# Kernel optimization log

Hardware: AMD Instinct MI355X
Metric: run time of the kernel (lower is better)

Reference implementation:

```python
import jax, jax.numpy as jnp
import numpy as np

N, E = 20000, 320000
IN, HID, R, HEADS = 128, 256, 4, 4
C = HID // HEADS  # per-head dim


def setup_inputs() -> dict:
    key = jax.random.key(0)
    ks = jax.random.split(key, 20)
    g = lambda k, s, sc=0.05: jax.random.normal(k, s, jnp.float32) * sc
    return {
        'x': g(ks[0], (N, IN), 1.0),
        'edge_index': jax.random.randint(ks[1], (2, E), 0, N),
        'edge_type': jax.random.randint(ks[2], (E,), 0, R),
        'h_prev': g(ks[3], (N, HID), 1.0),
        # RGCN layer 1: relation weights, root weight, bias
        'W1': g(ks[4], (R, IN, HID)), 'root1': g(ks[5], (IN, HID)), 'b1': jnp.zeros((HID,), jnp.float32),
        # RGCN layer 2
        'W2': g(ks[6], (R, HID, HID)), 'root2': g(ks[7], (HID, HID)), 'b2': jnp.zeros((HID,), jnp.float32),
        # TransformerConv linears (query/key/value/skip), each Linear(HID, HEADS*C)
        'Wq': g(ks[8], (HID, HID)), 'bq': jnp.zeros((HID,), jnp.float32),
        'Wk': g(ks[9], (HID, HID)), 'bk': jnp.zeros((HID,), jnp.float32),
        'Wv': g(ks[10], (HID, HID)), 'bv': jnp.zeros((HID,), jnp.float32),
        'Wskip': g(ks[11], (HID, HID)), 'bskip': jnp.zeros((HID,), jnp.float32),
        # GRUCell (torch layout: [3*HID, in], gates ordered r, z, n)
        'W_ih': g(ks[12], (3 * HID, HID)), 'b_ih': jnp.zeros((3 * HID,), jnp.float32),
        'W_hh': g(ks[13], (3 * HID, HID)), 'b_hh': jnp.zeros((3 * HID,), jnp.float32),
    }


def rgcn(x, src, dst, etype, W, Wroot, b):
    # PyG RGCNConv: out_i = x_i @ Wroot + b + sum_r mean_{j in N_r(i)} x_j @ W_r
    n = x.shape[0]
    out = x @ Wroot + b
    xs = x[src]  # [E, F_in]
    for r in range(W.shape[0]):  # small fixed relation count
        mask = (etype == r).astype(x.dtype)  # [E]
        msg = (xs @ W[r]) * mask[:, None]  # [E, F_out]
        agg = jax.ops.segment_sum(msg, dst, num_segments=n)
        cnt = jax.ops.segment_sum(mask, dst, num_segments=n)
        out = out + agg / jnp.maximum(cnt, 1.0)[:, None]
    return out


def transformer_conv(x, src, dst, Wq, bq, Wk, bk, Wv, bv, Wskip, bskip):
    # PyG TransformerConv, concat=True, root_weight=True
    n = x.shape[0]
    q = (x @ Wq + bq).reshape(n, HEADS, C)
    k = (x @ Wk + bk).reshape(n, HEADS, C)
    v = (x @ Wv + bv).reshape(n, HEADS, C)
    score = jnp.einsum('ehc,ehc->eh', q[dst], k[src]) * (1.0 / np.sqrt(C))  # [E, H]
    smax = jax.ops.segment_max(score, dst, num_segments=n)  # [N, H]
    ex = jnp.exp(score - smax[dst])
    denom = jax.ops.segment_sum(ex, dst, num_segments=n)
    alpha = ex / jnp.maximum(denom[dst], 1e-16)  # edge softmax per dst node
    out = jax.ops.segment_sum(alpha[:, :, None] * v[src], dst, num_segments=n)  # [N, H, C]
    return out.reshape(n, HEADS * C) + x @ Wskip + bskip


def gru_cell(xi, h, W_ih, b_ih, W_hh, b_hh):
    gi = xi @ W_ih.T + b_ih
    gh = h @ W_hh.T + b_hh
    ir, iz, inn = jnp.split(gi, 3, axis=1)
    hr, hz, hn = jnp.split(gh, 3, axis=1)
    r = jax.nn.sigmoid(ir + hr)
    z = jax.nn.sigmoid(iz + hz)
    nw = jnp.tanh(inn + r * hn)
    return (1.0 - z) * nw + z * h


def reference(x, edge_index, edge_type, h_prev, W1, root1, b1, W2, root2, b2,
              Wq, bq, Wk, bk, Wv, bv, Wskip, bskip, W_ih, b_ih, W_hh, b_hh):
    src, dst = edge_index[0], edge_index[1]
    h = jax.nn.relu(rgcn(x, src, dst, edge_type, W1, root1, b1))
    h = jax.nn.relu(rgcn(h, src, dst, edge_type, W2, root2, b2))
    h = transformer_conv(h, src, dst, Wq, bq, Wk, bk, Wv, bv, Wskip, bskip)
    h = gru_cell(h, h_prev, W_ih, b_ih, W_hh, b_hh)
    return h
```

## Files before the change

kernel.cpp:

```cpp
#include <hip/hip_runtime.h>
#include <hip/hip_bf16.h>
#include <stdint.h>

#define N_NODES 20000
#define E_EDGES 320000
#define IN_F    128
#define HIDF    256
#define R_REL   4
#define NRKEYS  (N_NODES*R_REL)
#define SCAN_BLOCKS 80

typedef __attribute__((ext_vector_type(8))) short  short8;
typedef __attribute__((ext_vector_type(4))) float  floatx4;

__device__ __forceinline__ float bf2f(__hip_bfloat16 v){ return __bfloat162float(v); }
__device__ __forceinline__ __hip_bfloat16 f2bf(float v){ return __float2bfloat16(v); }
__device__ __forceinline__ float bfbits2f(unsigned short u){ return __uint_as_float(((unsigned)u)<<16); }
__device__ __forceinline__ unsigned short f2bfbits(float v){
    __hip_bfloat16 h = __float2bfloat16(v);
    return *(unsigned short*)&h;
}
__device__ __forceinline__ unsigned pack_bf2(float a, float b){
    return (unsigned)f2bfbits(a) | ((unsigned)f2bfbits(b) << 16);
}

__device__ __forceinline__ void gload_lds16(const void* g, void* l)
{
    __builtin_amdgcn_global_load_lds((const __attribute__((address_space(1))) void*)g,
                                     (__attribute__((address_space(3))) void*)l, 16, 0, 0);
}

template<int N>
__device__ __forceinline__ void wait_vm()
{
    if constexpr (N == 0)      asm volatile("s_waitcnt vmcnt(0)" ::: "memory");
    else if constexpr (N == 3) asm volatile("s_waitcnt vmcnt(3)" ::: "memory");
    else if constexpr (N == 4) asm volatile("s_waitcnt vmcnt(4)" ::: "memory");
    else if constexpr (N == 5) asm volatile("s_waitcnt vmcnt(5)" ::: "memory");
    else if constexpr (N == 8) asm volatile("s_waitcnt vmcnt(8)" ::: "memory");
    else                       asm volatile("s_waitcnt vmcnt(0)" ::: "memory");
}

__device__ __forceinline__ int2 xcd_swizzle()
{
    int gx = gridDim.x, gy = gridDim.y;
    int nwg = gx * gy;
    int lin = blockIdx.x + gx * blockIdx.y;
    int q = nwg >> 3, r = nwg & 7;
    int k = lin & 7, i = lin >> 3;
    int j = (k < r ? k*(q+1) : r*(q+1) + (k-r)*q) + i;
    return make_int2(j / gy, j % gy);
}

__global__ void count_kernel(const int* __restrict__ ei, const int* __restrict__ et,
                             int* __restrict__ cnt)
{
    int e = blockIdx.x*256 + threadIdx.x;
    if (e >= E_EDGES) return;
    int dst = ei[E_EDGES + e];
    atomicAdd(&cnt[dst*R_REL + et[e]], 1);
}

__global__ __launch_bounds__(1024) void scan_reduce_kernel(const int* __restrict__ cnt,
                                                           int* __restrict__ blocksum)
{
    int ix = blockIdx.x*1024 + threadIdx.x;
    int v = (ix < NRKEYS) ? cnt[ix] : 0;
    #pragma unroll
    for (int o=32;o>0;o>>=1) v += __shfl_xor(v, o, 64);
    __shared__ int wsum[16];
    int wave = threadIdx.x >> 6, lane = threadIdx.x & 63;
    if (lane == 0) wsum[wave] = v;
    __syncthreads();
    if (threadIdx.x == 0) {
        int s = 0;
        #pragma unroll
        for (int w=0;w<16;w++) s += wsum[w];
        blocksum[blockIdx.x] = s;
    }
}

__global__ __launch_bounds__(128) void scan_sums_kernel(const int* __restrict__ blocksum,
                                                        int* __restrict__ blockoff)
{
    __shared__ int s[128];
    int t = threadIdx.x;
    int v = (t < SCAN_BLOCKS) ? blocksum[t] : 0;
    s[t] = v; __syncthreads();
    for (int off=1; off<128; off<<=1) {
        int u = (t>=off) ? s[t-off] : 0;
        __syncthreads();
        s[t] += u;
        __syncthreads();
    }
    if (t < SCAN_BLOCKS) blockoff[t] = s[t] - v;
}

__global__ __launch_bounds__(1024) void scan_apply_kernel(const int* __restrict__ cnt,
                                                          const int* __restrict__ blockoff,
                                                          int* __restrict__ row_ptr,
                                                          int* __restrict__ cursor)
{
    __shared__ int s[1024];
    int t = threadIdx.x;
    int ix = blockIdx.x*1024 + t;
    int v = (ix < NRKEYS) ? cnt[ix] : 0;
    s[t] = v; __syncthreads();
    for (int off=1; off<1024; off<<=1) {
        int u = (t>=off) ? s[t-off] : 0;
        __syncthreads();
        s[t] += u;
        __syncthreads();
    }
    if (ix < NRKEYS) {
        int excl = blockoff[blockIdx.x] + s[t] - v;
        row_ptr[ix] = excl;
        cursor[ix]  = excl;
        if (ix == NRKEYS-1) row_ptr[NRKEYS] = excl + v;
    }
}

__global__ void fill_kernel(const int* __restrict__ ei, const int* __restrict__ et,
                            int* __restrict__ cursor, int* __restrict__ csr_src)
{
    int e = blockIdx.x*256 + threadIdx.x;
    if (e >= E_EDGES) return;
    int src = ei[e];
    int dst = ei[E_EDGES + e];
    int key = dst*R_REL + et[e];
    int pos = atomicAdd(&cursor[key], 1);
    csr_src[pos] = src;
}

__global__ void make_b1t(const float* __restrict__ root1,
                         const float* __restrict__ W1,
                         __hip_bfloat16* __restrict__ B1t)
{
    int idx = blockIdx.x*256 + threadIdx.x;
    if (idx >= 256*640) return;
    int n = idx / 640, k = idx % 640;
    float v;
    if (k < 128) v = root1[k*256 + n];
    else         v = W1[(k-128)*256 + n];
    B1t[idx] = f2bf(v);
}

__global__ void make_b2t(const float* __restrict__ root2,
                         const float* __restrict__ W2,
                         __hip_bfloat16* __restrict__ B2t)
{
    int idx = blockIdx.x*256 + threadIdx.x;
    if (idx >= 256*1280) return;
    int n = idx / 1280, k = idx % 1280;
    float v;
    if (k < 256) v = root2[k*256 + n];
    else         v = W2[(k-256)*256 + n];
    B2t[idx] = f2bf(v);
}

__global__ void make_b3t(const float* __restrict__ Wq, const float* __restrict__ Wk,
                         const float* __restrict__ Wv, const float* __restrict__ Wsk,
                         const float* __restrict__ bq, const float* __restrict__ bk,
                         const float* __restrict__ bv, const float* __restrict__ bsk,
                         __hip_bfloat16* __restrict__ B3t, float* __restrict__ bias3)
{
    int idx = blockIdx.x*256 + threadIdx.x;
    if (idx >= 1024*256) return;
    int n = idx / 256, k = idx % 256;
    int g = n >> 8, nn = n & 255;
    const float* W = (g==0)?Wq:(g==1)?Wk:(g==2)?Wv:Wsk;
    B3t[idx] = f2bf(W[k*256 + nn]);
    if (k == 0) {
        const float* B = (g==0)?bq:(g==1)?bk:(g==2)?bv:bsk;
        bias3[n] = B[nn];
    }
}

__global__ void cvt_f32_bf16(const float* __restrict__ in, __hip_bfloat16* __restrict__ out, int n)
{
    int i = blockIdx.x*256 + threadIdx.x;
    if (i < n) out[i] = f2bf(in[i]);
}

__global__ __launch_bounds__(256) void agg1_kernel(const float* __restrict__ x,
                                                   const int* __restrict__ row_ptr,
                                                   const int* __restrict__ csr_src,
                                                   __hip_bfloat16* __restrict__ A1)
{
    int b = blockIdx.x*4 + (threadIdx.x >> 6);
    int lane = threadIdx.x & 63;
    int i = b >> 2, r = b & 3;
    int e0 = row_ptr[b], e1 = row_ptr[b+1];
    float sx0=0.f,sy0=0.f, sx1=0.f,sy1=0.f, sx2=0.f,sy2=0.f, sx3=0.f,sy3=0.f;
    int e = e0;
    for (; e+4 <= e1; e += 4) {
        int i0=csr_src[e], i1=csr_src[e+1], i2=csr_src[e+2], i3=csr_src[e+3];
        float2 v0 = *(const float2*)(x + (size_t)i0*IN_F + lane*2);
        float2 v1 = *(const float2*)(x + (size_t)i1*IN_F + lane*2);
        float2 v2 = *(const float2*)(x + (size_t)i2*IN_F + lane*2);
        float2 v3 = *(const float2*)(x + (size_t)i3*IN_F + lane*2);
        sx0+=v0.x; sy0+=v0.y; sx1+=v1.x; sy1+=v1.y;
        sx2+=v2.x; sy2+=v2.y; sx3+=v3.x; sy3+=v3.y;
    }
    for (; e < e1; e++) {
        int i0 = csr_src[e];
        float2 v = *(const float2*)(x + (size_t)i0*IN_F + lane*2);
        sx0+=v.x; sy0+=v.y;
    }
    float sx = (sx0+sx1)+(sx2+sx3);
    float sy = (sy0+sy1)+(sy2+sy3);
    float inv = (e1>e0) ? 1.f/(float)(e1-e0) : 0.f;
    *(unsigned*)(A1 + (size_t)i*640 + 128 + r*128 + lane*2) = pack_bf2(sx*inv, sy*inv);
    if (r == 0) {
        float2 v = *(const float2*)(x + (size_t)i*IN_F + lane*2);
        *(unsigned*)(A1 + (size_t)i*640 + lane*2) = pack_bf2(v.x, v.y);
    }
}

__global__ __launch_bounds__(256) void agg2_kernel(const int* __restrict__ row_ptr,
                                                   const int* __restrict__ csr_src,
                                                   __hip_bfloat16* __restrict__ A2)
{
    int b = blockIdx.x*4 + (threadIdx.x >> 6);
    int lane = threadIdx.x & 63;
    int i = b >> 2, r = b & 3;
    int e0 = row_ptr[b], e1 = row_ptr[b+1];
    float a0=0.f,a1=0.f,a2=0.f,a3=0.f;
    float b0=0.f,b1=0.f,b2=0.f,b3=0.f;
    float c0=0.f,c1=0.f,c2=0.f,c3=0.f;
    float d0=0.f,d1=0.f,d2=0.f,d3=0.f;
    int e = e0;
    for (; e+4 <= e1; e += 4) {
        int i0=csr_src[e], i1=csr_src[e+1], i2=csr_src[e+2], i3=csr_src[e+3];
        ushort4 u0 = *(const ushort4*)(A2 + (size_t)i0*1280 + lane*4);
        ushort4 u1 = *(const ushort4*)(A2 + (size_t)i1*1280 + lane*4);
        ushort4 u2 = *(const ushort4*)(A2 + (size_t)i2*1280 + lane*4);
        ushort4 u3 = *(const ushort4*)(A2 + (size_t)i3*1280 + lane*4);
        a0+=bfbits2f(u0.x); a1+=bfbits2f(u0.y); a2+=bfbits2f(u0.z); a3+=bfbits2f(u0.w);
        b0+=bfbits2f(u1.x); b1+=bfbits2f(u1.y); b2+=bfbits2f(u1.z); b3+=bfbits2f(u1.w);
        c0+=bfbits2f(u2.x); c1+=bfbits2f(u2.y); c2+=bfbits2f(u2.z); c3+=bfbits2f(u2.w);
        d0+=bfbits2f(u3.x); d1+=bfbits2f(u3.y); d2+=bfbits2f(u3.z); d3+=bfbits2f(u3.w);
    }
    for (; e < e1; e++) {
        int i0 = csr_src[e];
        ushort4 u = *(const ushort4*)(A2 + (size_t)i0*1280 + lane*4);
        a0+=bfbits2f(u.x); a1+=bfbits2f(u.y); a2+=bfbits2f(u.z); a3+=bfbits2f(u.w);
    }
    float s0=(a0+b0)+(c0+d0), s1=(a1+b1)+(c1+d1), s2=(a2+b2)+(c2+d2), s3=(a3+b3)+(c3+d3);
    float inv = (e1>e0) ? 1.f/(float)(e1-e0) : 0.f;
    uint2 w;
    w.x = pack_bf2(s0*inv, s1*inv);
    w.y = pack_bf2(s2*inv, s3*inv);
    *(uint2*)(A2 + (size_t)i*1280 + 256 + r*256 + lane*4) = w;
}

template<int MI>
__device__ __forceinline__ void gemm_bt_body(const __hip_bfloat16* __restrict__ A, int lda,
                                             const __hip_bfloat16* __restrict__ Bt,
                                             const float* __restrict__ bias,
                                             __hip_bfloat16* __restrict__ C, int ldc,
                                             int M, int K, int relu,
                                             int tile_m, int tile_n,
                                             __hip_bfloat16* lds_a, __hip_bfloat16* lds_b)
{
    constexpr int A_ELEMS = MI*1024;
    constexpr int B_ELEMS = 4096;
    constexpr int L = MI/2 + 2;
    const int tid  = threadIdx.x;
    const int wave = tid >> 6;
    const int lane = tid & 63;
    const int wm = wave >> 1, wn = wave & 1;
    const int fm = lane & 15;
    const int q  = lane >> 4;
    const int sw = (q ^ ((fm >> 1) & 3)) * 8;

    floatx4 acc[MI][4];
    #pragma unroll
    for (int i=0;i<MI;i++)
        #pragma unroll
        for (int j=0;j<4;j++) acc[i][j] = (floatx4){0.f,0.f,0.f,0.f};

    const int srow   = lane >> 2;
    const int schunk = lane & 3;
    size_t a_goff[MI/2];
    #pragma unroll
    for (int s = 0; s < MI/2; ++s) {
        int r = (s*4 + wave)*16 + srow;
        int c = schunk ^ ((r >> 1) & 3);
        a_goff[s] = (size_t)min(tile_m + r, M-1)*lda + c*8;
    }
    size_t b_goff[2];
    #pragma unroll
    for (int s = 0; s < 2; ++s) {
        int r = (s*4 + wave)*16 + srow;
        int c = schunk ^ ((r >> 1) & 3);
        b_goff[s] = (size_t)(tile_n + r)*K + c*8;
    }

    const int nt = K >> 5;

    auto issue = [&](int t, int bufi) {
        const int kn = t << 5;
        #pragma unroll
        for (int s = 0; s < MI/2; ++s)
            gload_lds16(A + a_goff[s] + kn, lds_a + bufi*A_ELEMS + (s*4 + wave)*512);
        #pragma unroll
        for (int s = 0; s < 2; ++s)
            gload_lds16(Bt + b_goff[s] + kn, lds_b + bufi*B_ELEMS + (s*4 + wave)*512);
    };

    issue(0, 0);
    if (nt > 1) { issue(1, 1); wait_vm<L>(); }
    else        { wait_vm<0>(); }
    __builtin_amdgcn_s_barrier();

    int cur = 0, nx2 = 2;
    for (int t = 0; t < nt; ++t) {
        if (t + 2 < nt) issue(t + 2, nx2);

        const __hip_bfloat16* la = lds_a + cur*A_ELEMS;
        const __hip_bfloat16* lb = lds_b + cur*B_ELEMS;
        short8 afr[MI], bfr[4];
        #pragma unroll
        for (int i=0;i<MI;i++)
            afr[i] = *(const short8*)(la + (wm*(MI*16) + i*16 + fm)*32 + sw);
        #pragma unroll
        for (int j=0;j<4;j++)
            bfr[j] = *(const short8*)(lb + (wn*64 + j*16 + fm)*32 + sw);

        __builtin_amdgcn_s_setprio(1);
        #pragma unroll
        for (int i=0;i<MI;i++)
            #pragma unroll
            for (int j=0;j<4;j++)
                acc[i][j] = __builtin_amdgcn_mfma_f32_16x16x32_bf16(afr[i], bfr[j], acc[i][j], 0,0,0);
        __builtin_amdgcn_s_setprio(0);

        if (t + 1 < nt) {
            if (t + 2 < nt) wait_vm<L>();
            else            wait_vm<0>();
            __builtin_amdgcn_s_barrier();
            cur = (cur == 2) ? 0 : cur + 1;
            nx2 = (nx2 == 2) ? 0 : nx2 + 1;
        }
    }

    const int crow_base = tile_m + wm*(MI*16);
    const int ccol_base = tile_n + wn*64;
    #pragma unroll
    for (int i=0;i<MI;i++) {
        #pragma unroll
        for (int j=0;j<4;j++) {
            int c  = ccol_base + j*16 + fm;
            float bb = bias[c];
            #pragma unroll
            for (int rg=0; rg<4; rg++) {
                int r = crow_base + i*16 + q*4 + rg;
                if (r < M) {
                    float v = acc[i][j][rg] + bb;
                    if (relu) v = fmaxf(v, 0.f);
                    C[(size_t)r*ldc + c] = f2bf(v);
                }
            }
        }
    }
}

template<int MI>
__global__ __launch_bounds__(256) void gemm_bt_t(const __hip_bfloat16* __restrict__ A, int lda,
                                                 const __hip_bfloat16* __restrict__ Bt,
                                                 const float* __restrict__ bias,
                                                 __hip_bfloat16* __restrict__ C, int ldc,
                                                 int M, int K, int relu)
{
    __shared__ __align__(16) __hip_bfloat16 lds_a[3*MI*1024];
    __shared__ __align__(16) __hip_bfloat16 lds_b[3*4096];
    int2 xy = xcd_swizzle();
    gemm_bt_body<MI>(A, lda, Bt, bias, C, ldc, M, K, relu,
                     xy.x*(MI*32), xy.y*128, lds_a, lds_b);
}

__global__ __launch_bounds__(256) void gemm_gru_fused(
    const __hip_bfloat16* __restrict__ A0,
    const __hip_bfloat16* __restrict__ A1,
    const __hip_bfloat16* __restrict__ Bt0,
    const __hip_bfloat16* __restrict__ Bt1,
    const float* __restrict__ b_ih, const float* __restrict__ b_hh,
    const float* __restrict__ hprev, float* __restrict__ out)
{
    constexpr int BUF_ELEMS = 16384;
    __shared__ __align__(16) __hip_bfloat16 lds[2*BUF_ELEMS];
    int2 xy = xcd_swizzle();
    const int tile_m = xy.x * 64;
    const int c0     = xy.y * 64;
    const int tid = threadIdx.x, wave = tid >> 6, lane = tid & 63;
    const int wm = wave >> 1, wn = wave & 1;
    const int fm = lane & 15, q = lane >> 4;
    const int sw = (q ^ ((fm >> 1) & 3)) * 8;

    const int sub = lane >> 2, ch = lane & 3;
    const __hip_bfloat16* gsrc[8];
    int dstoff[8];
    #pragma unroll
    for (int s = 0; s < 8; ++s) {
        int seg = wave*8 + s;
        if (seg < 8) {
            int fr = seg*16 + sub;
            int mat = fr >> 6, rl = fr & 63;
            int c = ch ^ ((fr >> 1) & 3);
            int grow = min(tile_m + rl, N_NODES-1);
            gsrc[s] = (mat ? A1 : A0) + (size_t)grow*256 + c*8;
            dstoff[s] = seg*512;
        } else {
            int fs = seg - 8;
            int fr = fs*16 + sub;
            int grp = fr >> 6, ri = fr & 63;
            int mat = grp >= 3, gate = mat ? grp-3 : grp;
            int c = ch ^ ((fr >> 1) & 3);
            int grow = gate*256 + c0 + ri;
            gsrc[s] = (mat ? Bt1 : Bt0) + (size_t)grow*256 + c*8;
            dstoff[s] = 4096 + fs*512;
        }
    }

    floatx4 acc[2][3][2][2];
    #pragma unroll
    for (int m=0;m<2;m++)
        #pragma unroll
        for (int g=0;g<3;g++)
            #pragma unroll
            for (int i=0;i<2;i++)
                #pragma unroll
                for (int f=0;f<2;f++) acc[m][g][i][f] = (floatx4){0.f,0.f,0.f,0.f};

    auto issue = [&](int t, int bufi) {
        const int kn = t << 5;
        #pragma unroll
        for (int s = 0; s < 8; ++s)
            gload_lds16(gsrc[s] + kn, lds + bufi*BUF_ELEMS + dstoff[s]);
    };

    issue(0, 0);
    issue(1, 1);
    wait_vm<8>();
    __builtin_amdgcn_s_barrier();

    #pragma unroll 1
    for (int t = 0; t < 8; ++t) {
        const __hip_bfloat16* lb = lds + (t & 1)*BUF_ELEMS;
        short8 af[2][2], bfr[2][3][2];
        #pragma unroll
        for (int m=0;m<2;m++)
            #pragma unroll
            for (int i=0;i<2;i++)
                af[m][i] = *(const short8*)(lb + (m*64 + wm*32 + i*16 + fm)*32 + sw);
        #pragma unroll
        for (int m=0;m<2;m++)
            #pragma unroll
            for (int g=0;g<3;g++)
                #pragma unroll
                for (int f=0;f<2;f++)
                    bfr[m][g][f] = *(const short8*)(lb + 4096 + (((m*3+g)*64 + wn*32 + f*16 + fm)*32) + sw);

        __builtin_amdgcn_s_setprio(1);
        #pragma unroll
        for (int m=0;m<2;m++)
            #pragma unroll
            for (int g=0;g<3;g++)
                #pragma unroll
                for (int i=0;i<2;i++)
                    #pragma unroll
                    for (int f=0;f<2;f++)
                        acc[m][g][i][f] = __builtin_amdgcn_mfma_f32_16x16x32_bf16(af[m][i], bfr[m][g][f], acc[m][g][i][f], 0,0,0);
        __builtin_amdgcn_s_setprio(0);

        if (t + 1 < 8) {
            __builtin_amdgcn_s_barrier();
            if (t + 2 < 8) { issue(t + 2, t & 1); wait_vm<8>(); }
            else           wait_vm<0>();
            __builtin_amdgcn_s_barrier();
        }
    }

    #pragma unroll
    for (int f=0; f<2; ++f) {
        int c = c0 + wn*32 + f*16 + fm;
        float bir = b_ih[c], biz = b_ih[256+c], bin = b_ih[512+c];
        float bhr = b_hh[c], bhz = b_hh[256+c], bhn = b_hh[512+c];
        #pragma unroll
        for (int i=0; i<2; ++i) {
            #pragma unroll
            for (int rg=0; rg<4; ++rg) {
                int r = tile_m + wm*32 + i*16 + q*4 + rg;
                if (r < N_NODES) {
                    float gir = acc[0][0][i][f][rg] + bir;
                    float giz = acc[0][1][i][f][rg] + biz;
                    float gin = acc[0][2][i][f][rg] + bin;
                    float ghr = acc[1][0][i][f][rg] + bhr;
                    float ghz = acc[1][1][i][f][rg] + bhz;
                    float ghn = acc[1][2][i][f][rg] + bhn;
                    float rr = 1.f/(1.f + __expf(-(gir + ghr)));
                    float zz = 1.f/(1.f + __expf(-(giz + ghz)));
                    float xn = gin + rr*ghn;
                    float e2 = __expf(xn + xn);
                    float nn = 1.f - 2.f/(e2 + 1.f);
                    float h  = hprev[(size_t)r*256 + c];
                    out[(size_t)r*256 + c] = (1.f - zz)*nn + zz*h;
                }
            }
        }
    }
}

__global__ __launch_bounds__(256) void score_kernel(const __hip_bfloat16* __restrict__ qkvs,
                                                    const int* __restrict__ row_ptr,
                                                    const int* __restrict__ csr_src,
                                                    float* __restrict__ score)
{
    int i = blockIdx.x*4 + (threadIdx.x >> 6);
    int lane = threadIdx.x & 63;
    int h = lane >> 4, d4 = lane & 15;
    int e0 = row_ptr[i*R_REL], e1 = row_ptr[i*R_REL + R_REL];
    ushort4 qv = *(const ushort4*)(qkvs + (size_t)i*1024 + lane*4);
    float qx=bfbits2f(qv.x), qy=bfbits2f(qv.y), qz=bfbits2f(qv.z), qw=bfbits2f(qv.w);
    float* sp = score + (size_t)h*E_EDGES;
    int j = e0;
    for (; j+2 <= e1; j += 2) {
        int s0 = csr_src[j], s1 = csr_src[j+1];
        ushort4 k0 = *(const ushort4*)(qkvs + (size_t)s0*1024 + 256 + lane*4);
        ushort4 k1 = *(const ushort4*)(qkvs + (size_t)s1*1024 + 256 + lane*4);
        float d0 = qx*bfbits2f(k0.x)+qy*bfbits2f(k0.y)+qz*bfbits2f(k0.z)+qw*bfbits2f(k0.w);
        float d1 = qx*bfbits2f(k1.x)+qy*bfbits2f(k1.y)+qz*bfbits2f(k1.z)+qw*bfbits2f(k1.w);
        #pragma unroll
        for (int o=1;o<16;o<<=1){ d0 += __shfl_xor(d0,o,64); d1 += __shfl_xor(d1,o,64); }
        if (d4 == 0) { sp[j] = d0*0.125f; sp[j+1] = d1*0.125f; }
    }
    for (; j < e1; j++) {
        int s0 = csr_src[j];
        ushort4 k0 = *(const ushort4*)(qkvs + (size_t)s0*1024 + 256 + lane*4);
        float d0 = qx*bfbits2f(k0.x)+qy*bfbits2f(k0.y)+qz*bfbits2f(k0.z)+qw*bfbits2f(k0.w);
        #pragma unroll
        for (int o=1;o<16;o<<=1) d0 += __shfl_xor(d0,o,64);
        if (d4 == 0) sp[j] = d0*0.125f;
    }
}

__global__ __launch_bounds__(256) void attn_agg_kernel(const __hip_bfloat16* __restrict__ qkvs,
                                                       const float* __restrict__ score,
                                                       const int* __restrict__ row_ptr,
                                                       const int* __restrict__ csr_src,
                                                       __hip_bfloat16* __restrict__ hatt)
{
    int i = blockIdx.x*4 + (threadIdx.x >> 6);
    int lane = threadIdx.x & 63;
    int h  = lane >> 4;
    int d4 = lane & 15;
    int e0 = row_ptr[i*R_REL], e1 = row_ptr[i*R_REL + R_REL];
    int deg = e1 - e0;
    const float* sp = score + (size_t)h*E_EDGES + e0;

    float m = -1e30f;
    for (int j = d4; j < deg; j += 16) m = fmaxf(m, sp[j]);
    #pragma unroll
    for (int o=1;o<16;o<<=1) m = fmaxf(m, __shfl_xor(m, o, 64));

    float ssum = 0.f;
    for (int j = d4; j < deg; j += 16) ssum += __expf(sp[j] - m);
    #pragma unroll
    for (int o=1;o<16;o<<=1) ssum += __shfl_xor(ssum, o, 64);
    float inv = 1.f / fmaxf(ssum, 1e-16f);

    float ax=0.f, ay=0.f, az=0.f, aw=0.f;
    int j = 0;
    for (; j+4 <= deg; j += 4) {
        int s0=csr_src[e0+j], s1=csr_src[e0+j+1], s2=csr_src[e0+j+2], s3=csr_src[e0+j+3];
        float w0 = __expf(sp[j]   - m) * inv;
        float w1 = __expf(sp[j+1] - m) * inv;
        float w2 = __expf(sp[j+2] - m) * inv;
        float w3 = __expf(sp[j+3] - m) * inv;
        ushort4 u0 = *(const ushort4*)(qkvs + (size_t)s0*1024 + 512 + lane*4);
        ushort4 u1 = *(const ushort4*)(qkvs + (size_t)s1*1024 + 512 + lane*4);
        ushort4 u2 = *(const ushort4*)(qkvs + (size_t)s2*1024 + 512 + lane*4);
        ushort4 u3 = *(const ushort4*)(qkvs + (size_t)s3*1024 + 512 + lane*4);
        ax += w0*bfbits2f(u0.x) + w1*bfbits2f(u1.x) + w2*bfbits2f(u2.x) + w3*bfbits2f(u3.x);
        ay += w0*bfbits2f(u0.y) + w1*bfbits2f(u1.y) + w2*bfbits2f(u2.y) + w3*bfbits2f(u3.y);
        az += w0*bfbits2f(u0.z) + w1*bfbits2f(u1.z) + w2*bfbits2f(u2.z) + w3*bfbits2f(u3.z);
        aw += w0*bfbits2f(u0.w) + w1*bfbits2f(u1.w) + w2*bfbits2f(u2.w) + w3*bfbits2f(u3.w);
    }
    for (; j < deg; j++) {
        int s = csr_src[e0+j];
        float w = __expf(sp[j] - m) * inv;
        ushort4 u = *(const ushort4*)(qkvs + (size_t)s*1024 + 512 + lane*4);
        ax += w*bfbits2f(u.x); ay += w*bfbits2f(u.y);
        az += w*bfbits2f(u.z); aw += w*bfbits2f(u.w);
    }
    ushort4 sk = *(const ushort4*)(qkvs + (size_t)i*1024 + 768 + lane*4);
    uint2 w;
    w.x = pack_bf2(ax + bfbits2f(sk.x), ay + bfbits2f(sk.y));
    w.y = pack_bf2(az + bfbits2f(sk.z), aw + bfbits2f(sk.w));
    *(uint2*)(hatt + (size_t)i*256 + lane*4) = w;
}

extern "C" void kernel_launch(void* const* d_in, const int* in_sizes, int n_in,
                              void* d_out, int out_size, void* d_ws, size_t ws_size,
                              hipStream_t stream)
{
    const float* x       = (const float*)d_in[0];
    const int* edge_index= (const int*)d_in[1];
    const int* edge_type = (const int*)d_in[2];
    const float* hprev   = (const float*)d_in[3];
    const float* W1      = (const float*)d_in[4];
    const float* root1   = (const float*)d_in[5];
    const float* b1      = (const float*)d_in[6];
    const float* W2      = (const float*)d_in[7];
    const float* root2   = (const float*)d_in[8];
    const float* b2      = (const float*)d_in[9];
    const float* Wq      = (const float*)d_in[10];
    const float* bq      = (const float*)d_in[11];
    const float* Wk      = (const float*)d_in[12];
    const float* bk      = (const float*)d_in[13];
    const float* Wv      = (const float*)d_in[14];
    const float* bv      = (const float*)d_in[15];
    const float* Wskip   = (const float*)d_in[16];
    const float* bskip   = (const float*)d_in[17];
    const float* W_ih    = (const float*)d_in[18];
    const float* b_ih    = (const float*)d_in[19];
    const float* W_hh    = (const float*)d_in[20];
    const float* b_hh    = (const float*)d_in[21];

    char* ws = (char*)d_ws;
    size_t off = 0;
    auto take = [&](size_t bytes)->char* {
        char* p = ws + off;
        off = (off + bytes + 255) & ~(size_t)255;
        return p;
    };
    int* cnt        = (int*)take((size_t)NRKEYS*4);
    int* row_ptr    = (int*)take((size_t)(NRKEYS+1)*4);
    int* cursor     = (int*)take((size_t)NRKEYS*4);
    int* csr_src    = (int*)take((size_t)E_EDGES*4);
    int* blocksum   = (int*)take((size_t)SCAN_BLOCKS*4);
    int* blockoff   = (int*)take((size_t)(SCAN_BLOCKS+1)*4);
    float* score    = (float*)take((size_t)R_REL*E_EDGES*4);
    __hip_bfloat16* B1t   = (__hip_bfloat16*)take((size_t)256*640*2);
    __hip_bfloat16* B2t   = (__hip_bfloat16*)take((size_t)256*1280*2);
    __hip_bfloat16* B3t   = (__hip_bfloat16*)take((size_t)1024*256*2);
    __hip_bfloat16* Biht  = (__hip_bfloat16*)take((size_t)768*256*2);
    __hip_bfloat16* Bhht  = (__hip_bfloat16*)take((size_t)768*256*2);
    float*          bias3 = (float*)take((size_t)1024*4);
    __hip_bfloat16* hprev_bf = (__hip_bfloat16*)take((size_t)N_NODES*256*2);
    char* P1 = take((size_t)N_NODES*640*2);
    char* P2 = take((size_t)N_NODES*1536*2);

    __hip_bfloat16* A1   = (__hip_bfloat16*)P1;
    __hip_bfloat16* h2   = (__hip_bfloat16*)P1;
    __hip_bfloat16* hatt = (__hip_bfloat16*)P1;
    __hip_bfloat16* A2   = (__hip_bfloat16*)P2;
    __hip_bfloat16* qkvs = (__hip_bfloat16*)P2;

    hipMemsetAsync(cnt, 0, (size_t)NRKEYS*4, stream);
    count_kernel<<<(E_EDGES+255)/256, 256, 0, stream>>>(edge_index, edge_type, cnt);
    scan_reduce_kernel<<<SCAN_BLOCKS, 1024, 0, stream>>>(cnt, blocksum);
    scan_sums_kernel<<<1, 128, 0, stream>>>(blocksum, blockoff);
    scan_apply_kernel<<<SCAN_BLOCKS, 1024, 0, stream>>>(cnt, blockoff, row_ptr, cursor);
    fill_kernel<<<(E_EDGES+255)/256, 256, 0, stream>>>(edge_index, edge_type, cursor, csr_src);

    make_b1t<<<(256*640+255)/256, 256, 0, stream>>>(root1, W1, B1t);
    make_b2t<<<(256*1280+255)/256, 256, 0, stream>>>(root2, W2, B2t);
    make_b3t<<<(1024*256+255)/256, 256, 0, stream>>>(Wq, Wk, Wv, Wskip, bq, bk, bv, bskip, B3t, bias3);
    cvt_f32_bf16<<<(768*256+255)/256, 256, 0, stream>>>(W_ih, Biht, 768*256);
    cvt_f32_bf16<<<(768*256+255)/256, 256, 0, stream>>>(W_hh, Bhht, 768*256);
    cvt_f32_bf16<<<(N_NODES*256+255)/256, 256, 0, stream>>>(hprev, hprev_bf, N_NODES*256);

    agg1_kernel<<<NRKEYS/4, 256, 0, stream>>>(x, row_ptr, csr_src, A1);

    dim3 g12(313, 2);
    gemm_bt_t<2><<<g12, 256, 0, stream>>>(A1, 640, B1t, b1, A2, 1280, N_NODES, 640, 1);

    agg2_kernel<<<NRKEYS/4, 256, 0, stream>>>(row_ptr, csr_src, A2);

    gemm_bt_t<2><<<g12, 256, 0, stream>>>(A2, 1280, B2t, b2, h2, 256, N_NODES, 1280, 1);

    dim3 g3(157, 8);
    gemm_bt_t<4><<<g3, 256, 0, stream>>>(h2, 256, B3t, bias3, qkvs, 1024, N_NODES, 256, 0);

    score_kernel<<<N_NODES/4, 256, 0, stream>>>(qkvs, row_ptr, csr_src, score);
    attn_agg_kernel<<<N_NODES/4, 256, 0, stream>>>(qkvs, score, row_ptr, csr_src, hatt);

    gemm_gru_fused<<<dim3(313, 4), 256, 0, stream>>>(hatt, hprev_bf, Biht, Bhht,
                                                     b_ih, b_hh, hprev, (float*)d_out);
}
```

Baseline: 426.4 us.

## Fuse attention score and aggregation with online softmax, bf16 gather, larger GRU tiles

The separate score and attention-aggregation kernels become one kernel that computes an online softmax per destination node, removing the score buffer round trip and a launch. agg1 now gathers from a bf16 copy of x made by an extra conversion kernel, halving gather bytes at the cost of that pass and some precision. The fused GRU GEMM moves to 512 threads with 128-row tiles and a reworked load split, so fewer blocks each do more work. The online softmax rescales its accumulators when the running max grows, which adds some exp calls per edge.

After: 415.6 us. 1.03x faster.

```diff
diff --git a/kernel.cpp b/kernel.cpp
--- a/kernel.cpp
+++ b/kernel.cpp
@@ -37,7 +37,6 @@
     else if constexpr (N == 3) asm volatile("s_waitcnt vmcnt(3)" ::: "memory");
     else if constexpr (N == 4) asm volatile("s_waitcnt vmcnt(4)" ::: "memory");
     else if constexpr (N == 5) asm volatile("s_waitcnt vmcnt(5)" ::: "memory");
-    else if constexpr (N == 8) asm volatile("s_waitcnt vmcnt(8)" ::: "memory");
     else                       asm volatile("s_waitcnt vmcnt(0)" ::: "memory");
 }
 
@@ -182,7 +181,7 @@
     if (i < n) out[i] = f2bf(in[i]);
 }
 
-__global__ __launch_bounds__(256) void agg1_kernel(const float* __restrict__ x,
+__global__ __launch_bounds__(256) void agg1_kernel(const __hip_bfloat16* __restrict__ xbf,
                                                    const int* __restrict__ row_ptr,
                                                    const int* __restrict__ csr_src,
                                                    __hip_bfloat16* __restrict__ A1)
@@ -195,26 +194,26 @@
     int e = e0;
     for (; e+4 <= e1; e += 4) {
         int i0=csr_src[e], i1=csr_src[e+1], i2=csr_src[e+2], i3=csr_src[e+3];
-        float2 v0 = *(const float2*)(x + (size_t)i0*IN_F + lane*2);
-        float2 v1 = *(const float2*)(x + (size_t)i1*IN_F + lane*2);
-        float2 v2 = *(const float2*)(x + (size_t)i2*IN_F + lane*2);
-        float2 v3 = *(const float2*)(x + (size_t)i3*IN_F + lane*2);
-        sx0+=v0.x; sy0+=v0.y; sx1+=v1.x; sy1+=v1.y;
-        sx2+=v2.x; sy2+=v2.y; sx3+=v3.x; sy3+=v3.y;
+        unsigned u0 = *(const unsigned*)(xbf + (size_t)i0*IN_F + lane*2);
+        unsigned u1 = *(const unsigned*)(xbf + (size_t)i1*IN_F + lane*2);
+        unsigned u2 = *(const unsigned*)(xbf + (size_t)i2*IN_F + lane*2);
+        unsigned u3 = *(const unsigned*)(xbf + (size_t)i3*IN_F + lane*2);
+        sx0+=bfbits2f((unsigned short)u0); sy0+=bfbits2f((unsigned short)(u0>>16));
+        sx1+=bfbits2f((unsigned short)u1); sy1+=bfbits2f((unsigned short)(u1>>16));
+        sx2+=bfbits2f((unsigned short)u2); sy2+=bfbits2f((unsigned short)(u2>>16));
+        sx3+=bfbits2f((unsigned short)u3); sy3+=bfbits2f((unsigned short)(u3>>16));
     }
     for (; e < e1; e++) {
         int i0 = csr_src[e];
-        float2 v = *(const float2*)(x + (size_t)i0*IN_F + lane*2);
-        sx0+=v.x; sy0+=v.y;
+        unsigned u = *(const unsigned*)(xbf + (size_t)i0*IN_F + lane*2);
+        sx0+=bfbits2f((unsigned short)u); sy0+=bfbits2f((unsigned short)(u>>16));
     }
     float sx = (sx0+sx1)+(sx2+sx3);
     float sy = (sy0+sy1)+(sy2+sy3);
     float inv = (e1>e0) ? 1.f/(float)(e1-e0) : 0.f;
     *(unsigned*)(A1 + (size_t)i*640 + 128 + r*128 + lane*2) = pack_bf2(sx*inv, sy*inv);
-    if (r == 0) {
-        float2 v = *(const float2*)(x + (size_t)i*IN_F + lane*2);
-        *(unsigned*)(A1 + (size_t)i*640 + lane*2) = pack_bf2(v.x, v.y);
-    }
+    if (r == 0)
+        *(unsigned*)(A1 + (size_t)i*640 + lane*2) = *(const unsigned*)(xbf + (size_t)i*IN_F + lane*2);
 }
 
 __global__ __launch_bounds__(256) void agg2_kernel(const int* __restrict__ row_ptr,
@@ -380,7 +379,7 @@
                      xy.x*(MI*32), xy.y*128, lds_a, lds_b);
 }
 
-__global__ __launch_bounds__(256) void gemm_gru_fused(
+__global__ __launch_bounds__(512) void gemm_gru_fused(
     const __hip_bfloat16* __restrict__ A0,
     const __hip_bfloat16* __restrict__ A1,
     const __hip_bfloat16* __restrict__ Bt0,
@@ -388,10 +387,10 @@
     const float* __restrict__ b_ih, const float* __restrict__ b_hh,
     const float* __restrict__ hprev, float* __restrict__ out)
 {
-    constexpr int BUF_ELEMS = 16384;
+    constexpr int BUF_ELEMS = 20480;
     __shared__ __align__(16) __hip_bfloat16 lds[2*BUF_ELEMS];
     int2 xy = xcd_swizzle();
-    const int tile_m = xy.x * 64;
+    const int tile_m = xy.x * 128;
     const int c0     = xy.y * 64;
     const int tid = threadIdx.x, wave = tid >> 6, lane = tid & 63;
     const int wm = wave >> 1, wn = wave & 1;
@@ -399,27 +398,27 @@
     const int sw = (q ^ ((fm >> 1) & 3)) * 8;
 
     const int sub = lane >> 2, ch = lane & 3;
-    const __hip_bfloat16* gsrc[8];
-    int dstoff[8];
-    #pragma unroll
-    for (int s = 0; s < 8; ++s) {
-        int seg = wave*8 + s;
-        if (seg < 8) {
+    const __hip_bfloat16* gsrc[5];
+    int dstoff[5];
+    #pragma unroll
+    for (int s = 0; s < 5; ++s) {
+        int seg = wave*5 + s;
+        if (seg < 16) {
             int fr = seg*16 + sub;
-            int mat = fr >> 6, rl = fr & 63;
+            int mat = fr >> 7, rl = fr & 127;
             int c = ch ^ ((fr >> 1) & 3);
             int grow = min(tile_m + rl, N_NODES-1);
             gsrc[s] = (mat ? A1 : A0) + (size_t)grow*256 + c*8;
             dstoff[s] = seg*512;
         } else {
-            int fs = seg - 8;
+            int fs = seg - 16;
             int fr = fs*16 + sub;
             int grp = fr >> 6, ri = fr & 63;
             int mat = grp >= 3, gate = mat ? grp-3 : grp;
             int c = ch ^ ((fr >> 1) & 3);
             int grow = gate*256 + c0 + ri;
             gsrc[s] = (mat ? Bt1 : Bt0) + (size_t)grow*256 + c*8;
-            dstoff[s] = 4096 + fs*512;
+            dstoff[s] = 8192 + fs*512;
         }
     }
 
@@ -436,13 +435,13 @@
     auto issue = [&](int t, int bufi) {
         const int kn = t << 5;
         #pragma unroll
-        for (int s = 0; s < 8; ++s)
+        for (int s = 0; s < 5; ++s)
             gload_lds16(gsrc[s] + kn, lds + bufi*BUF_ELEMS + dstoff[s]);
     };
 
     issue(0, 0);
     issue(1, 1);
-    wait_vm<8>();
+    wait_vm<5>();
     __builtin_amdgcn_s_barrier();
 
     #pragma unroll 1
@@ -453,14 +452,14 @@
         for (int m=0;m<2;m++)
             #pragma unroll
             for (int i=0;i<2;i++)
-                af[m][i] = *(const short8*)(lb + (m*64 + wm*32 + i*16 + fm)*32 + sw);
+                af[m][i] = *(const short8*)(lb + (m*128 + wm*32 + i*16 + fm)*32 + sw);
         #pragma unroll
         for (int m=0;m<2;m++)
             #pragma unroll
             for (int g=0;g<3;g++)
                 #pragma unroll
                 for (int f=0;f<2;f++)
-                    bfr[m][g][f] = *(const short8*)(lb + 4096 + (((m*3+g)*64 + wn*32 + f*16 + fm)*32) + sw);
+                    bfr[m][g][f] = *(const short8*)(lb + 8192 + (((m*3+g)*64 + wn*32 + f*16 + fm)*32) + sw);
 
         __builtin_amdgcn_s_setprio(1);
         #pragma unroll
@@ -476,7 +475,7 @@
 
         if (t + 1 < 8) {
             __builtin_amdgcn_s_barrier();
-            if (t + 2 < 8) { issue(t + 2, t & 1); wait_vm<8>(); }
+            if (t + 2 < 8) { issue(t + 2, t & 1); wait_vm<5>(); }
             else           wait_vm<0>();
             __builtin_amdgcn_s_barrier();
         }
@@ -512,92 +511,74 @@
     }
 }
 
-__global__ __launch_bounds__(256) void score_kernel(const __hip_bfloat16* __restrict__ qkvs,
-                                                    const int* __restrict__ row_ptr,
-                                                    const int* __restrict__ csr_src,
-                                                    float* __restrict__ score)
+__global__ __launch_bounds__(256) void attn_fused_kernel(
+    const __hip_bfloat16* __restrict__ qkvs,
+    const int* __restrict__ row_ptr,
+    const int* __restrict__ csr_src,
+    __hip_bfloat16* __restrict__ hatt)
 {
     int i = blockIdx.x*4 + (threadIdx.x >> 6);
     int lane = threadIdx.x & 63;
-    int h = lane >> 4, d4 = lane & 15;
     int e0 = row_ptr[i*R_REL], e1 = row_ptr[i*R_REL + R_REL];
+
     ushort4 qv = *(const ushort4*)(qkvs + (size_t)i*1024 + lane*4);
     float qx=bfbits2f(qv.x), qy=bfbits2f(qv.y), qz=bfbits2f(qv.z), qw=bfbits2f(qv.w);
-    float* sp = score + (size_t)h*E_EDGES;
+
+    float m = -1e30f, denom = 0.f;
+    float ax=0.f, ay=0.f, az=0.f, aw=0.f;
+
     int j = e0;
     for (; j+2 <= e1; j += 2) {
         int s0 = csr_src[j], s1 = csr_src[j+1];
-        ushort4 k0 = *(const ushort4*)(qkvs + (size_t)s0*1024 + 256 + lane*4);
-        ushort4 k1 = *(const ushort4*)(qkvs + (size_t)s1*1024 + 256 + lane*4);
+        const __hip_bfloat16* r0 = qkvs + (size_t)s0*1024;
+        const __hip_bfloat16* r1 = qkvs + (size_t)s1*1024;
+        ushort4 k0 = *(const ushort4*)(r0 + 256 + lane*4);
+        ushort4 k1 = *(const ushort4*)(r1 + 256 + lane*4);
+        ushort4 v0 = *(const ushort4*)(r0 + 512 + lane*4);
+        ushort4 v1 = *(const ushort4*)(r1 + 512 + lane*4);
         float d0 = qx*bfbits2f(k0.x)+qy*bfbits2f(k0.y)+qz*bfbits2f(k0.z)+qw*bfbits2f(k0.w);
         float d1 = qx*bfbits2f(k1.x)+qy*bfbits2f(k1.y)+qz*bfbits2f(k1.z)+qw*bfbits2f(k1.w);
         #pragma unroll
         for (int o=1;o<16;o<<=1){ d0 += __shfl_xor(d0,o,64); d1 += __shfl_xor(d1,o,64); }
-        if (d4 == 0) { sp[j] = d0*0.125f; sp[j+1] = d1*0.125f; }
-    }
-    for (; j < e1; j++) {
+        d0 *= 0.125f; d1 *= 0.125f;
+        float mx = fmaxf(d0, d1);
+        if (mx > m) {
+            float sc = __expf(m - mx);
+            ax*=sc; ay*=sc; az*=sc; aw*=sc; denom*=sc;
+            m = mx;
+        }
+        float w0 = __expf(d0 - m), w1 = __expf(d1 - m);
+        denom += w0 + w1;
+        ax += w0*bfbits2f(v0.x) + w1*bfbits2f(v1.x);
+        ay += w0*bfbits2f(v0.y) + w1*bfbits2f(v1.y);
+        az += w0*bfbits2f(v0.z) + w1*bfbits2f(v1.z);
+        aw += w0*bfbits2f(v0.w) + w1*bfbits2f(v1.w);
+    }
+    for (; j < e1; ++j) {
         int s0 = csr_src[j];
-        ushort4 k0 = *(const ushort4*)(qkvs + (size_t)s0*1024 + 256 + lane*4);
+        const __hip_bfloat16* r0 = qkvs + (size_t)s0*1024;
+        ushort4 k0 = *(const ushort4*)(r0 + 256 + lane*4);
+        ushort4 v0 = *(const ushort4*)(r0 + 512 + lane*4);
         float d0 = qx*bfbits2f(k0.x)+qy*bfbits2f(k0.y)+qz*bfbits2f(k0.z)+qw*bfbits2f(k0.w);
         #pragma unroll
         for (int o=1;o<16;o<<=1) d0 += __shfl_xor(d0,o,64);
-        if (d4 == 0) sp[j] = d0*0.125f;
-    }
-}
-
-__global__ __launch_bounds__(256) void attn_agg_kernel(const __hip_bfloat16* __restrict__ qkvs,
-                                                       const float* __restrict__ score,
-                                                       const int* __restrict__ row_ptr,
-                                                       const int* __restrict__ csr_src,
-                                                       __hip_bfloat16* __restrict__ hatt)
-{
-    int i = blockIdx.x*4 + (threadIdx.x >> 6);
-    int lane = threadIdx.x & 63;
-    int h  = lane >> 4;
-    int d4 = lane & 15;
-    int e0 = row_ptr[i*R_REL], e1 = row_ptr[i*R_REL + R_REL];
-    int deg = e1 - e0;
-    const float* sp = score + (size_t)h*E_EDGES + e0;
-
-    float m = -1e30f;
-    for (int j = d4; j < deg; j += 16) m = fmaxf(m, sp[j]);
-    #pragma unroll
-    for (int o=1;o<16;o<<=1) m = fmaxf(m, __shfl_xor(m, o, 64));
-
-    float ssum = 0.f;
-    for (int j = d4; j < deg; j += 16) ssum += __expf(sp[j] - m);
-    #pragma unroll
-    for (int o=1;o<16;o<<=1) ssum += __shfl_xor(ssum, o, 64);
-    float inv = 1.f / fmaxf(ssum, 1e-16f);
-
-    float ax=0.f, ay=0.f, az=0.f, aw=0.f;
-    int j = 0;
-    for (; j+4 <= deg; j += 4) {
-        int s0=csr_src[e0+j], s1=csr_src[e0+j+1], s2=csr_src[e0+j+2], s3=csr_src[e0+j+3];
-        float w0 = __expf(sp[j]   - m) * inv;
-        float w1 = __expf(sp[j+1] - m) * inv;
-        float w2 = __expf(sp[j+2] - m) * inv;
-        float w3 = __expf(sp[j+3] - m) * inv;
-        ushort4 u0 = *(const ushort4*)(qkvs + (size_t)s0*1024 + 512 + lane*4);
-        ushort4 u1 = *(const ushort4*)(qkvs + (size_t)s1*1024 + 512 + lane*4);
-        ushort4 u2 = *(const ushort4*)(qkvs + (size_t)s2*1024 + 512 + lane*4);
-        ushort4 u3 = *(const ushort4*)(qkvs + (size_t)s3*1024 + 512 + lane*4);
-        ax += w0*bfbits2f(u0.x) + w1*bfbits2f(u1.x) + w2*bfbits2f(u2.x) + w3*bfbits2f(u3.x);
-        ay += w0*bfbits2f(u0.y) + w1*bfbits2f(u1.y) + w2*bfbits2f(u2.y) + w3*bfbits2f(u3.y);
-        az += w0*bfbits2f(u0.z) + w1*bfbits2f(u1.z) + w2*bfbits2f(u2.z) + w3*bfbits2f(u3.z);
-        aw += w0*bfbits2f(u0.w) + w1*bfbits2f(u1.w) + w2*bfbits2f(u2.w) + w3*bfbits2f(u3.w);
-    }
-    for (; j < deg; j++) {
-        int s = csr_src[e0+j];
-        float w = __expf(sp[j] - m) * inv;
-        ushort4 u = *(const ushort4*)(qkvs + (size_t)s*1024 + 512 + lane*4);
-        ax += w*bfbits2f(u.x); ay += w*bfbits2f(u.y);
-        az += w*bfbits2f(u.z); aw += w*bfbits2f(u.w);
-    }
+        d0 *= 0.125f;
+        if (d0 > m) {
+            float sc = __expf(m - d0);
+            ax*=sc; ay*=sc; az*=sc; aw*=sc; denom*=sc;
+            m = d0;
+        }
+        float w0 = __expf(d0 - m);
+        denom += w0;
+        ax += w0*bfbits2f(v0.x); ay += w0*bfbits2f(v0.y);
+        az += w0*bfbits2f(v0.z); aw += w0*bfbits2f(v0.w);
+    }
+
+    float inv = 1.f / fmaxf(denom, 1e-16f);
     ushort4 sk = *(const ushort4*)(qkvs + (size_t)i*1024 + 768 + lane*4);
     uint2 w;
-    w.x = pack_bf2(ax + bfbits2f(sk.x), ay + bfbits2f(sk.y));
-    w.y = pack_bf2(az + bfbits2f(sk.z), aw + bfbits2f(sk.w));
+    w.x = pack_bf2(ax*inv + bfbits2f(sk.x), ay*inv + bfbits2f(sk.y));
+    w.y = pack_bf2(az*inv + bfbits2f(sk.z), aw*inv + bfbits2f(sk.w));
     *(uint2*)(hatt + (size_t)i*256 + lane*4) = w;
 }
 
@@ -641,7 +622,6 @@
     int* csr_src    = (int*)take((size_t)E_EDGES*4);
     int* blocksum   = (int*)take((size_t)SCAN_BLOCKS*4);
     int* blockoff   = (int*)take((size_t)(SCAN_BLOCKS+1)*4);
-    float* score    = (float*)take((size_t)R_REL*E_EDGES*4);
     __hip_bfloat16* B1t   = (__hip_bfloat16*)take((size_t)256*640*2);
     __hip_bfloat16* B2t   = (__hip_bfloat16*)take((size_t)256*1280*2);
     __hip_bfloat16* B3t   = (__hip_bfloat16*)take((size_t)1024*256*2);
@@ -649,6 +629,7 @@
     __hip_bfloat16* Bhht  = (__hip_bfloat16*)take((size_t)768*256*2);
     float*          bias3 = (float*)take((size_t)1024*4);
     __hip_bfloat16* hprev_bf = (__hip_bfloat16*)take((size_t)N_NODES*256*2);
+    __hip_bfloat16* xbf      = (__hip_bfloat16*)take((size_t)N_NODES*IN_F*2);
     char* P1 = take((size_t)N_NODES*640*2);
     char* P2 = take((size_t)N_NODES*1536*2);
 
@@ -671,8 +652,9 @@
     cvt_f32_bf16<<<(768*256+255)/256, 256, 0, stream>>>(W_ih, Biht, 768*256);
     cvt_f32_bf16<<<(768*256+255)/256, 256, 0, stream>>>(W_hh, Bhht, 768*256);
     cvt_f32_bf16<<<(N_NODES*256+255)/256, 256, 0, stream>>>(hprev, hprev_bf, N_NODES*256);
-
-    agg1_kernel<<<NRKEYS/4, 256, 0, stream>>>(x, row_ptr, csr_src, A1);
+    cvt_f32_bf16<<<(N_NODES*IN_F+255)/256, 256, 0, stream>>>(x, xbf, N_NODES*IN_F);
+
+    agg1_kernel<<<NRKEYS/4, 256, 0, stream>>>(xbf, row_ptr, csr_src, A1);
 
     dim3 g12(313, 2);
     gemm_bt_t<2><<<g12, 256, 0, stream>>>(A1, 640, B1t, b1, A2, 1280, N_NODES, 640, 1);
@@ -684,9 +666,8 @@
     dim3 g3(157, 8);
     gemm_bt_t<4><<<g3, 256, 0, stream>>>(h2, 256, B3t, bias3, qkvs, 1024, N_NODES, 256, 0);
 
-    score_kernel<<<N_NODES/4, 256, 0, stream>>>(qkvs, row_ptr, csr_src, score);
-    attn_agg_kernel<<<N_NODES/4, 256, 0, stream>>>(qkvs, score, row_ptr, csr_src, hatt);
-
-    gemm_gru_fused<<<dim3(313, 4), 256, 0, stream>>>(hatt, hprev_bf, Biht, Bhht,
+    attn_fused_kernel<<<N_NODES/4, 256, 0, stream>>>(qkvs, row_ptr, csr_src, hatt);
+
+    gemm_gru_fused<<<dim3(157, 4), 512, 0, stream>>>(hatt, hprev_bf, Biht, Bhht,
                                                      b_ih, b_hh, hprev, (float*)d_out);
 }
```
